# Kernel tuning notes

Hardware: AMD Instinct MI355X
Metric: run time of the kernel (lower is better)

## Reference

```python
import jax, jax.numpy as jnp
import numpy as np

U, I, D = 100000, 50000, 64
N = U + I
E_G, E_U, E_I = 2400000, 1600000, 800000


def _spmm(rows, cols, vals, x, n):
    # sparse [n, m] @ dense [m, d] via gather + scale + segment-sum scatter
    return jax.ops.segment_sum(x[cols] * vals[:, None], rows, num_segments=n)


def setup_inputs() -> dict:
    key = jax.random.key(0)
    ks = jax.random.split(key, 11)
    return {
        "user_emb": jax.random.normal(ks[0], (U, D), dtype=jnp.float32),
        "item_emb": jax.random.normal(ks[1], (I, D), dtype=jnp.float32),
        "graph_rows": jax.random.randint(ks[2], (E_G,), 0, N, dtype=jnp.int32),
        "graph_cols": jax.random.randint(ks[3], (E_G,), 0, N, dtype=jnp.int32),
        "graph_vals": jax.random.uniform(ks[4], (E_G,), dtype=jnp.float32),
        "user_rows": jax.random.randint(ks[5], (E_U,), 0, U, dtype=jnp.int32),
        "user_cols": jax.random.randint(ks[6], (E_U,), 0, U, dtype=jnp.int32),
        "user_vals": jax.random.uniform(ks[7], (E_U,), dtype=jnp.float32),
        "item_rows": jax.random.randint(ks[8], (E_I,), 0, I, dtype=jnp.int32),
        "item_cols": jax.random.randint(ks[9], (E_I,), 0, I, dtype=jnp.int32),
        "item_vals": jax.random.uniform(ks[10], (E_I,), dtype=jnp.float32),
    }


def reference(user_emb, item_emb,
              graph_rows, graph_cols, graph_vals,
              user_rows, user_cols, user_vals,
              item_rows, item_cols, item_vals):
    all_emb = jnp.concatenate([user_emb, item_emb], axis=0)  # [N, D]
    all_emb1 = _spmm(graph_rows, graph_cols, graph_vals, all_emb, N)
    user_emb2 = _spmm(user_rows, user_cols, user_vals, user_emb, U)
    item_emb2 = _spmm(item_rows, item_cols, item_vals, item_emb, I)
    user_emb1, item_emb1 = all_emb1[:U], all_emb1[U:]
    return (user_emb1, item_emb1, user_emb2, item_emb2)
```

## Files before the change

kernel.cpp:

```cpp
#include <hip/hip_runtime.h>

#define DDIM 64
constexpr int U_CNT = 100000;
constexpr int I_CNT = 50000;
constexpr int N_CNT = U_CNT + I_CNT;
constexpr int NB    = N_CNT + U_CNT + I_CNT;

constexpr int BIN_ROWS_LOG = 8;
constexpr int BIN_ROWS = 1 << BIN_ROWS_LOG;
constexpr int BINS = (NB + BIN_ROWS - 1) / BIN_ROWS;
constexpr int BINS_PAD = 1536;
constexpr int SORT_EDGES = 4096;
constexpr int HIST_EDGES = 16384;
constexpr int CAP = 4672;
constexpr int NSLOT = 10;

constexpr int SB_LOG = 12;
constexpr int NSB = (NB + (1 << SB_LOG) - 1) >> SB_LOG;
constexpr int NSB_PAD = 128;
constexpr int BWIN = 48;

typedef unsigned u32x2 __attribute__((ext_vector_type(2)));
typedef unsigned u32x4 __attribute__((ext_vector_type(4)));

__device__ __forceinline__ int wave_incl_scan(int v, int lane) {
#pragma unroll
    for (int off = 1; off < 64; off <<= 1) {
        int t = __shfl_up(v, off, 64);
        if (lane >= off) v += t;
    }
    return v;
}

__device__ __forceinline__ unsigned short f2bf_rne(float f) {
    unsigned u = __float_as_uint(f);
    unsigned r = (u + 0x7FFFu + ((u >> 16) & 1u)) >> 16;
    return (unsigned short)r;
}

__global__ __launch_bounds__(256) void convert_emb(const float* __restrict__ ue,
                                                   const float* __restrict__ ie,
                                                   unsigned short* __restrict__ emb16) {
    int g = blockIdx.x * 256 + threadIdx.x;
    constexpr int UG = U_CNT * (DDIM / 4);
    constexpr int TG = N_CNT * (DDIM / 4);
    if (g >= TG) return;
    float4 v = (g < UG) ? ((const float4*)ue)[g] : ((const float4*)ie)[g - UG];
    ushort4 o;
    o.x = f2bf_rne(v.x); o.y = f2bf_rne(v.y); o.z = f2bf_rne(v.z); o.w = f2bf_rne(v.w);
    ((ushort4*)emb16)[g] = o;
}

__global__ __launch_bounds__(1024) void hist_conv(const int* __restrict__ gr,
                                                  const int* __restrict__ ur,
                                                  const int* __restrict__ ir,
                                                  int EG, int EU, int EI,
                                                  int* __restrict__ cnt,
                                                  const float* __restrict__ ue,
                                                  const float* __restrict__ ie,
                                                  unsigned short* __restrict__ emb16) {
    __shared__ int h[BINS_PAD];
    for (int i = threadIdx.x; i < BINS_PAD; i += 1024) h[i] = 0;

    if (emb16) {
        constexpr int UG = U_CNT * (DDIM / 4);
        constexpr int TG = N_CNT * (DDIM / 4);
        int stride = (int)gridDim.x * 1024;
        for (int g = blockIdx.x * 1024 + threadIdx.x; g < TG; g += stride) {
            float4 v = (g < UG) ? ((const float4*)ue)[g] : ((const float4*)ie)[g - UG];
            ushort4 o;
            o.x = f2bf_rne(v.x); o.y = f2bf_rne(v.y); o.z = f2bf_rne(v.z); o.w = f2bf_rne(v.w);
            ((ushort4*)emb16)[g] = o;
        }
    }
    __syncthreads();

    int base = blockIdx.x * HIST_EDGES;
    int Et = EG + EU + EI;
    for (int j = 0; j < HIST_EDGES / 1024; ++j) {
        int e = base + j * 1024 + threadIdx.x;
        if (e < Et) {
            int b;
            if (e < EG)           b = gr[e];
            else if (e < EG + EU) b = N_CNT + ur[e - EG];
            else                  b = N_CNT + U_CNT + ir[e - EG - EU];
            atomicAdd(&h[b >> BIN_ROWS_LOG], 1);
        }
    }
    __syncthreads();
    for (int i = threadIdx.x; i < BINS; i += 1024) {
        int v = h[i];
        if (v) atomicAdd(&cnt[i], v);
    }
}

__global__ __launch_bounds__(1024) void scan_bins(const int* __restrict__ cnt,
                                                  int* __restrict__ bin_base,
                                                  int* __restrict__ bin_cursor,
                                                  int* __restrict__ sb_base,
                                                  int* __restrict__ sb_cursor,
                                                  int E_total) {
    __shared__ int wsum[16], woff[16];
    int tid = threadIdx.x, lane = tid & 63, wid = tid >> 6;
    int i0 = 2 * tid, i1 = 2 * tid + 1;
    int c0 = (i0 < BINS) ? cnt[i0] : 0;
    int c1 = (i1 < BINS) ? cnt[i1] : 0;
    int v = c0 + c1;
    int incl = wave_incl_scan(v, lane);
    if (lane == 63) wsum[wid] = incl;
    __syncthreads();
    if (wid == 0 && lane < 16) {
        int s = wsum[lane], si = s;
#pragma unroll
        for (int off = 1; off < 16; off <<= 1) {
            int t = __shfl_up(si, off, 64);
            if (lane >= off) si += t;
        }
        woff[lane] = si - s;
    }
    __syncthreads();
    int e = incl - v + woff[wid];
    if (i0 < BINS) { bin_base[i0] = e;      bin_cursor[i0] = e; }
    if (i1 < BINS) { bin_base[i1] = e + c0; bin_cursor[i1] = e + c0; }
    if (tid == 0) bin_base[BINS] = E_total;
    if (sb_base) {
        __syncthreads();
        if (tid <= NSB) {
            int idx = tid << (SB_LOG - BIN_ROWS_LOG);
            int vv = (idx >= BINS) ? E_total : bin_base[idx];
            sb_base[tid] = vv;
            if (tid < NSB) sb_cursor[tid] = vv;
        }
    }
}

__global__ __launch_bounds__(512, 6) void sbsort_all(
        const int* __restrict__ gr, const int* __restrict__ gc, const float* __restrict__ gv,
        const int* __restrict__ ur, const int* __restrict__ uc, const float* __restrict__ uv,
        const int* __restrict__ ir, const int* __restrict__ ic, const float* __restrict__ iv,
        int EG, int EU, int EI,
        int* __restrict__ sb_cursor, uint2* __restrict__ poolA) {
    __shared__ uint2 sorted[SORT_EDGES];
    __shared__ unsigned char ssb[SORT_EDGES];
    __shared__ int hist[NSB_PAD];
    __shared__ int lscan[NSB_PAD];
    __shared__ int lcur[NSB_PAD];
    __shared__ int wsum2[2];

    int tid = threadIdx.x, lane = tid & 63, wid = tid >> 6;
    for (int i = tid; i < NSB_PAD; i += 512) { hist[i] = 0; lcur[i] = 0; }
    __syncthreads();

    const int Et = EG + EU + EI;
    int start = blockIdx.x * SORT_EDGES;
    int base_e = start + tid * 8;
    int myb[8]; unsigned mylo[8]; float myv[8];

#pragma unroll
    for (int j = 0; j < 8; j += 4) {
        int e = base_e + j;
        int sg0 = (e < EG) ? 0 : (e < EG + EU ? 1 : 2);
        int sg3 = (e + 3 < EG) ? 0 : (e + 3 < EG + EU ? 1 : 2);
        if (e + 3 < Et && sg0 == sg3) {
            const int* R; const int* Cc; const float* V; int boff, goff, loc;
            if (sg0 == 0)      { R = gr; Cc = gc; V = gv; boff = 0;             goff = 0;     loc = e; }
            else if (sg0 == 1) { R = ur; Cc = uc; V = uv; boff = N_CNT;         goff = 0;     loc = e - EG; }
            else               { R = ir; Cc = ic; V = iv; boff = N_CNT + U_CNT; goff = U_CNT; loc = e - EG - EU; }
            int4   r4 = *(const int4*)(R + loc);
            int4   c4 = *(const int4*)(Cc + loc);
            float4 v4 = *(const float4*)(V + loc);
            int rr[4] = {r4.x, r4.y, r4.z, r4.w};
            int cc[4] = {c4.x, c4.y, c4.z, c4.w};
            float vv[4] = {v4.x, v4.y, v4.z, v4.w};
#pragma unroll
            for (int q = 0; q < 4; ++q) {
                int bucket = boff + rr[q];
                int sb = bucket >> SB_LOG;
                myb[j + q] = sb;
                mylo[j + q] = ((unsigned)(bucket & 4095) << 18) | (unsigned)(goff + cc[q]);
                myv[j + q] = vv[q];
                atomicAdd(&hist[sb], 1);
            }
        } else {
#pragma unroll
            for (int q = 0; q < 4; ++q) {
                int ee = e + q;
                if (ee < Et) {
                    int r, c; float vl; int boff, goff;
                    if (ee < EG)           { r = gr[ee]; c = gc[ee]; vl = gv[ee]; boff = 0; goff = 0; }
                    else if (ee < EG + EU) { int k = ee - EG;      r = ur[k]; c = uc[k]; vl = uv[k]; boff = N_CNT;         goff = 0; }
                    else                   { int k = ee - EG - EU; r = ir[k]; c = ic[k]; vl = iv[k]; boff = N_CNT + U_CNT; goff = U_CNT; }
                    int bucket = boff + r;
                    int sb = bucket >> SB_LOG;
                    myb[j + q] = sb;
                    mylo[j + q] = ((unsigned)(bucket & 4095) << 18) | (unsigned)(goff + c);
                    myv[j + q] = vl;
                    atomicAdd(&hist[sb], 1);
                } else myb[j + q] = -1;
            }
        }
    }
    __syncthreads();

    int v = 0, incl = 0;
    if (tid < NSB_PAD) {
        v = hist[tid];
        incl = wave_incl_scan(v, lane);
        if (lane == 63) wsum2[wid] = incl;
    }
    __syncthreads();
    if (tid < NSB_PAD) {
        int st = incl - v + (wid ? wsum2[0] : 0);
        lscan[tid] = st;
        if (tid < NSB && v) hist[tid] = atomicAdd(&sb_cursor[tid], v);
    }
    __syncthreads();

#pragma unroll
    for (int j = 0; j < 8; ++j) {
        if (myb[j] >= 0) {
            int p = lscan[myb[j]] + atomicAdd(&lcur[myb[j]], 1);
            sorted[p] = make_uint2(mylo[j], __float_as_uint(myv[j]));
            ssb[p] = (unsigned char)myb[j];
        }
    }
    __syncthreads();

    int cntE = min(SORT_EDGES, Et - start);
    for (int pos = tid; pos < cntE; pos += 512) {
        int b = ssb[pos];
        uint2 t = sorted[pos];
        u32x2 q; q.x = t.x; q.y = t.y;
        __builtin_nontemporal_store(q, (u32x2*)&poolA[hist[b] + (pos - lscan[b])]);
    }
}

__global__ __launch_bounds__(512, 6) void binsort2(const uint2* __restrict__ poolA,
                                                   const int* __restrict__ sb_base, int Et,
                                                   int* __restrict__ bin_cursor,
                                                   uint2* __restrict__ poolB) {
    __shared__ uint2 sorted[SORT_EDGES];
    __shared__ unsigned char sbin[SORT_EDGES];
    __shared__ int hist[BWIN];
    __shared__ int lscan[BWIN];
    __shared__ int lcur[BWIN];
    __shared__ int ssbb[NSB + 1];
    __shared__ int W0s, nloc;

    int tid = threadIdx.x, lane = tid & 63;
    if (tid < BWIN) { hist[tid] = 0; }
    if (tid <= NSB) ssbb[tid] = sb_base[tid];
    __syncthreads();

    int start = blockIdx.x * SORT_EDGES;
    int base_e = start + tid * 8;
    int sb;
    {
        int lo2 = 0, hi2 = NSB - 1;
        while (lo2 < hi2) {
            int mid = (lo2 + hi2 + 1) >> 1;
            if (ssbb[mid] <= base_e) lo2 = mid; else hi2 = mid - 1;
        }
        sb = lo2;
    }
    if (tid == 0) W0s = sb << (SB_LOG - BIN_ROWS_LOG);
    __syncthreads();
    int W0 = W0s;

    int myb[8]; uint2 myp[8];
#pragma unroll
    for (int j = 0; j < 8; j += 2) {
        int e = base_e + j;
        uint2 p0, p1;
        bool v1 = (e + 1 < Et), v0 = (e < Et);
        if (v1) {
            u32x4 q = __builtin_nontemporal_load((const u32x4*)(poolA + e));
            p0.x = q.x; p0.y = q.y; p1.x = q.z; p1.y = q.w;
        } else if (v0) {
            u32x2 q = __builtin_nontemporal_load((const u32x2*)(poolA + e));
            p0.x = q.x; p0.y = q.y;
        }
        if (v0) {
            while (sb < NSB - 1 && e >= ssbb[sb + 1]) ++sb;
            int b = (sb << (SB_LOG - BIN_ROWS_LOG)) + (int)(p0.x >> 26);
            int slot = b - W0;
            if ((unsigned)slot < (unsigned)BWIN) {
                myb[j] = slot; myp[j] = p0;
                atomicAdd(&hist[slot], 1);
            } else {
                int gp = atomicAdd(&bin_cursor[b], 1);
                poolB[gp] = p0;
                myb[j] = -1;
            }
        } else myb[j] = -1;
        if (v1) {
            int e1 = e + 1;
            while (sb < NSB - 1 && e1 >= ssbb[sb + 1]) ++sb;
            int b = (sb << (SB_LOG - BIN_ROWS_LOG)) + (int)(p1.x >> 26);
            int slot = b - W0;
            if ((unsigned)slot < (unsigned)BWIN) {
                myb[j + 1] = slot; myp[j + 1] = p1;
                atomicAdd(&hist[slot], 1);
            } else {
                int gp = atomicAdd(&bin_cursor[b], 1);
                poolB[gp] = p1;
                myb[j + 1] = -1;
            }
        } else myb[j + 1] = -1;
    }
    __syncthreads();

    if (tid < 64) {
        int vv = (tid < BWIN) ? hist[tid] : 0;
        int incl = wave_incl_scan(vv, lane);
        if (tid < BWIN) { lscan[tid] = incl - vv; lcur[tid] = incl - vv; }
        if (tid == BWIN - 1) nloc = incl;
    }
    __syncthreads();
    if (tid < BWIN && hist[tid] > 0)
        hist[tid] = atomicAdd(&bin_cursor[W0 + tid], hist[tid]);
    __syncthreads();

#pragma unroll
    for (int j = 0; j < 8; ++j) {
        if (myb[j] >= 0) {
            int p = atomicAdd(&lcur[myb[j]], 1);
            sorted[p] = myp[j];
            sbin[p] = (unsigned char)myb[j];
        }
    }
    __syncthreads();

    int tot = nloc;
    for (int pos = tid; pos < tot; pos += 512) {
        int sl = sbin[pos];
        uint2 t = sorted[pos];
        u32x2 q; q.x = t.x; q.y = t.y;
        __builtin_nontemporal_store(q, (u32x2*)&poolB[hist[sl] + (pos - lscan[sl])]);
    }
}

__global__ __launch_bounds__(512) void binsort(const int* __restrict__ rows,
                                               const int* __restrict__ cols,
                                               const float* __restrict__ vals, int E,
                                               int bucket_base, int gidx_base,
                                               int* __restrict__ bin_cursor,
                                               uint2* __restrict__ pool) {
    __shared__ uint2 sorted[SORT_EDGES];
    __shared__ unsigned short sbin[SORT_EDGES];
    __shared__ int hist[BINS_PAD];
    __shared__ int lscan[BINS_PAD];
    __shared__ int lcur[BINS_PAD];
    __shared__ int wsum[8], woff[8];

    int tid = threadIdx.x, lane = tid & 63, wid = tid >> 6;
    for (int i = tid; i < BINS_PAD; i += 512) { hist[i] = 0; lcur[i] = 0; }
    __syncthreads();

    int start = blockIdx.x * SORT_EDGES;
    int base_e = start + tid * 8;
    int myb[8]; unsigned mylo[8]; float myv[8];
#pragma unroll
    for (int j = 0; j < 8; j += 4) {
        int e = base_e + j;
        if (e + 3 < E) {
            int4   r4 = *(const int4*)(rows + e);
            int4   c4 = *(const int4*)(cols + e);
            float4 v4 = *(const float4*)(vals + e);
            int rr[4] = {r4.x, r4.y, r4.z, r4.w};
            int cc[4] = {c4.x, c4.y, c4.z, c4.w};
            float vv[4] = {v4.x, v4.y, v4.z, v4.w};
#pragma unroll
            for (int q = 0; q < 4; ++q) {
                int bucket = bucket_base + rr[q];
                myb[j + q] = bucket >> BIN_ROWS_LOG;
                mylo[j + q] = ((unsigned)(bucket & (BIN_ROWS - 1)) << 18) |
                              (unsigned)(gidx_base + cc[q]);
                myv[j + q] = vv[q];
                atomicAdd(&hist[myb[j + q]], 1);
            }
        } else {
#pragma unroll
            for (int q = 0; q < 4; ++q) {
                int ee = e + q;
                if (ee < E) {
                    int bucket = bucket_base + rows[ee];
                    myb[j + q] = bucket >> BIN_ROWS_LOG;
                    mylo[j + q] = ((unsigned)(bucket & (BIN_ROWS - 1)) << 18) |
                                  (unsigned)(gidx_base + cols[ee]);
                    myv[j + q] = vals[ee];
                    atomicAdd(&hist[myb[j + q]], 1);
                } else myb[j + q] = -1;
            }
        }
    }
    __syncthreads();

    int s0 = 3 * tid, s1 = s0 + 1, s2 = s0 + 2;
    int h0 = hist[s0], h1 = hist[s1], h2 = hist[s2];
    int v = h0 + h1 + h2;
    int incl = wave_incl_scan(v, lane);
    if (lane == 63) wsum[wid] = incl;
    __syncthreads();
    if (wid == 0 && lane < 8) {
        int s = wsum[lane], si = s;
#pragma unroll
        for (int off = 1; off < 8; off <<= 1) {
            int t = __shfl_up(si, off, 64);
            if (lane >= off) si += t;
        }
        woff[lane] = si - s;
    }
    __syncthreads();
    int e0 = incl - v + woff[wid];
    lscan[s0] = e0; lscan[s1] = e0 + h0; lscan[s2] = e0 + h0 + h1;
    if (s0 < BINS && h0) hist[s0] = atomicAdd(&bin_cursor[s0], h0);
    if (s1 < BINS && h1) hist[s1] = atomicAdd(&bin_cursor[s1], h1);
    if (s2 < BINS && h2) hist[s2] = atomicAdd(&bin_cursor[s2], h2);
    __syncthreads();

#pragma unroll
    for (int j = 0; j < 8; ++j) {
        if (myb[j] >= 0) {
            int p = lscan[myb[j]] + atomicAdd(&lcur[myb[j]], 1);
            sorted[p] = make_uint2(mylo[j], __float_as_uint(myv[j]));
            sbin[p] = (unsigned short)myb[j];
        }
    }
    __syncthreads();

    int cntE = min(SORT_EDGES, E - start);
    for (int pos = tid; pos < cntE; pos += 512) {
        int b = sbin[pos];
        pool[hist[b] + (pos - lscan[b])] = sorted[pos];
    }
}

template <bool BF16>
__global__ __launch_bounds__(512, 8) void refine_accum(const int* __restrict__ bin_base,
                                                       const uint2* __restrict__ pool,
                                                       const unsigned short* __restrict__ emb16,
                                                       const float* __restrict__ ue,
                                                       const float* __restrict__ ie,
                                                       float* __restrict__ out) {
    __shared__ uint2 sorted[CAP];
    __shared__ int rhist[BIN_ROWS];
    __shared__ int rstart[BIN_ROWS];
    __shared__ int rcur[BIN_ROWS];
    __shared__ int wsum[4];
    int tid = threadIdx.x, lane = tid & 63, wid = tid >> 6;
    int b = blockIdx.x;
    int s = bin_base[b], e = bin_base[b + 1];
    int cnt = min(e - s, CAP);

    if (tid < BIN_ROWS) rhist[tid] = 0;
    __syncthreads();

    uint2 my[NSLOT];
    const u32x2* poolv = (const u32x2*)(pool + s);
#pragma unroll
    for (int j = 0; j < NSLOT; ++j) {
        int idx = tid + j * 512;
        if (idx < cnt) {
            u32x2 q = __builtin_nontemporal_load(poolv + idx);
            my[j].x = q.x; my[j].y = q.y;
            atomicAdd(&rhist[(q.x >> 18) & 255u], 1);
        }
    }
    __syncthreads();

    int v = 0, incl = 0;
    if (tid < BIN_ROWS) {
        v = rhist[tid];
        incl = wave_incl_scan(v, lane);
        if (lane == 63) wsum[wid] = incl;
    }
    __syncthreads();
    if (tid < BIN_ROWS) {
        int off = 0;
#pragma unroll
        for (int w = 0; w < 4; ++w)
            if (w < wid) off += wsum[w];
        int st = incl - v + off;
        rstart[tid] = st; rcur[tid] = st;
    }
    __syncthreads();

#pragma unroll
    for (int j = 0; j < NSLOT; ++j) {
        int idx = tid + j * 512;
        if (idx < cnt) {
            int pos = atomicAdd(&rcur[(my[j].x >> 18) & 255u], 1);
            sorted[pos] = my[j];
        }
    }
    __syncthreads();

    long long rowbase = (long long)b * BIN_ROWS;
    auto gather = [&](unsigned gi) -> float {
        if (BF16) return __uint_as_float((unsigned)emb16[(gi << 6) + lane] << 16);
        return (gi < (unsigned)U_CNT) ? ue[((size_t)gi << 6) + lane]
                                      : ie[(((size_t)gi - U_CNT) << 6) + lane];
    };
    for (int r = wid; r < BIN_ROWS; r += 8) {
        long long row = rowbase + r;
        if (row >= NB) break;
        int k = rstart[r], ke = k + rhist[r];
        float acc0 = 0.f, acc1 = 0.f;
        for (; k + 8 <= ke; k += 8) {
            uint2 p0 = sorted[k],     p1 = sorted[k + 1], p2 = sorted[k + 2], p3 = sorted[k + 3];
            uint2 p4 = sorted[k + 4], p5 = sorted[k + 5], p6 = sorted[k + 6], p7 = sorted[k + 7];
            float x0 = gather(p0.x & 0x3FFFFu);
            float x1 = gather(p1.x & 0x3FFFFu);
            float x2 = gather(p2.x & 0x3FFFFu);
            float x3 = gather(p3.x & 0x3FFFFu);
            float x4 = gather(p4.x & 0x3FFFFu);
            float x5 = gather(p5.x & 0x3FFFFu);
            float x6 = gather(p6.x & 0x3FFFFu);
            float x7 = gather(p7.x & 0x3FFFFu);
            acc0 += __uint_as_float(p0.y) * x0;
            acc1 += __uint_as_float(p1.y) * x1;
            acc0 += __uint_as_float(p2.y) * x2;
            acc1 += __uint_as_float(p3.y) * x3;
            acc0 += __uint_as_float(p4.y) * x4;
            acc1 += __uint_as_float(p5.y) * x5;
            acc0 += __uint_as_float(p6.y) * x6;
            acc1 += __uint_as_float(p7.y) * x7;
        }
        for (; k + 4 <= ke; k += 4) {
            uint2 p0 = sorted[k], p1 = sorted[k + 1], p2 = sorted[k + 2], p3 = sorted[k + 3];
            float x0 = gather(p0.x & 0x3FFFFu);
            float x1 = gather(p1.x & 0x3FFFFu);
            float x2 = gather(p2.x & 0x3FFFFu);
            float x3 = gather(p3.x & 0x3FFFFu);
            acc0 += __uint_as_float(p0.y) * x0;
            acc1 += __uint_as_float(p1.y) * x1;
            acc0 += __uint_as_float(p2.y) * x2;
            acc1 += __uint_as_float(p3.y) * x3;
        }
        for (; k < ke; ++k) {
            uint2 p = sorted[k];
            acc0 += __uint_as_float(p.y) * gather(p.x & 0x3FFFFu);
        }
        __builtin_nontemporal_store(acc0 + acc1, &out[(size_t)row * DDIM + lane]);
    }
}

__global__ void spmm_graph_kernel(const int* __restrict__ rows, const int* __restrict__ cols,
                                  const float* __restrict__ vals,
                                  const float* __restrict__ user_emb,
                                  const float* __restrict__ item_emb,
                                  float* __restrict__ out, int E) {
    long long idx = (long long)blockIdx.x * blockDim.x + threadIdx.x;
    int e = (int)(idx >> 6), d = (int)(idx & 63);
    if (e >= E) return;
    int r = rows[e], c = cols[e];
    float v = vals[e];
    float x = (c < U_CNT) ? user_emb[(long long)c * DDIM + d]
                          : item_emb[(long long)(c - U_CNT) * DDIM + d];
    atomicAdd(&out[(long long)r * DDIM + d], v * x);
}

__global__ void spmm_plain_kernel(const int* __restrict__ rows, const int* __restrict__ cols,
                                  const float* __restrict__ vals,
                                  const float* __restrict__ emb,
                                  float* __restrict__ out, int E) {
    long long idx = (long long)blockIdx.x * blockDim.x + threadIdx.x;
    int e = (int)(idx >> 6), d = (int)(idx & 63);
    if (e >= E) return;
    int r = rows[e], c = cols[e];
    atomicAdd(&out[(long long)r * DDIM + d], vals[e] * emb[(long long)c * DDIM + d]);
}

extern "C" void kernel_launch(void* const* d_in, const int* in_sizes, int n_in,
                              void* d_out, int out_size, void* d_ws, size_t ws_size,
                              hipStream_t stream) {
    const float* user_emb = (const float*)d_in[0];
    const float* item_emb = (const float*)d_in[1];
    const int*   g_rows   = (const int*)d_in[2];
    const int*   g_cols   = (const int*)d_in[3];
    const float* g_vals   = (const float*)d_in[4];
    const int*   u_rows   = (const int*)d_in[5];
    const int*   u_cols   = (const int*)d_in[6];
    const float* u_vals   = (const float*)d_in[7];
    const int*   i_rows   = (const int*)d_in[8];
    const int*   i_cols   = (const int*)d_in[9];
    const float* i_vals   = (const float*)d_in[10];
    float* out = (float*)d_out;

    const int EG = in_sizes[2];
    const int EU = in_sizes[5];
    const int EI = in_sizes[8];
    const int Et = EG + EU + EI;

    const size_t emb_bytes = (size_t)N_CNT * DDIM * sizeof(unsigned short);

    size_t t_off_bb   = (size_t)BINS_PAD * sizeof(int);
    size_t t_off_bc   = t_off_bb + (size_t)(BINS + 1) * sizeof(int);
    size_t t_off_sbb  = t_off_bc + (size_t)BINS * sizeof(int);
    size_t t_off_sbc  = t_off_sbb + (size_t)(NSB + 1) * sizeof(int);
    size_t t_off_pa   = (t_off_sbc + (size_t)NSB * sizeof(int) + 15) & ~(size_t)15;
    size_t t_off_pb   = t_off_pa + (size_t)Et * sizeof(uint2);
    size_t needed_2p  = t_off_pb + (size_t)Et * sizeof(uint2);
    size_t t_off_emb  = (needed_2p + 15) & ~(size_t)15;
    size_t needed_na  = t_off_emb + emb_bytes;
    bool pa_fits_emb  = (size_t)Et * sizeof(uint2) >= emb_bytes;

    size_t o_off_base   = (size_t)BINS_PAD * sizeof(int);
    size_t o_off_cursor = o_off_base + (size_t)(BINS + 1) * sizeof(int);
    size_t o_off_pool   = (o_off_cursor + (size_t)BINS * sizeof(int) + 15) & ~(size_t)15;
    size_t o_off_emb    = o_off_pool + (size_t)Et * sizeof(uint2);
    size_t needed_min   = o_off_emb;
    size_t needed_full  = o_off_emb + emb_bytes;

    if (ws_size >= needed_2p && pa_fits_emb) {
        bool noalias = (ws_size >= needed_na);
        int*   cnt        = (int*)d_ws;
        int*   bin_base   = (int*)((char*)d_ws + t_off_bb);
        int*   bin_cursor = (int*)((char*)d_ws + t_off_bc);
        int*   sb_base    = (int*)((char*)d_ws + t_off_sbb);
        int*   sb_cursor  = (int*)((char*)d_ws + t_off_sbc);
        uint2* poolA      = (uint2*)((char*)d_ws + t_off_pa);
        uint2* poolB      = (uint2*)((char*)d_ws + t_off_pb);
        unsigned short* emb16 = noalias ? (unsigned short*)((char*)d_ws + t_off_emb)
                                        : (unsigned short*)poolA;

        hipMemsetAsync(cnt, 0, (size_t)BINS_PAD * sizeof(int), stream);

        unsigned hblocks = (unsigned)((Et + HIST_EDGES - 1) / HIST_EDGES);
        hist_conv<<<hblocks, 1024, 0, stream>>>(g_rows, u_rows, i_rows, EG, EU, EI, cnt,
                                                user_emb, item_emb,
                                                noalias ? emb16 : (unsigned short*)nullptr);
        scan_bins<<<1, 1024, 0, stream>>>(cnt, bin_base, bin_cursor, sb_base, sb_cursor, Et);

        unsigned nb2 = (unsigned)((Et + SORT_EDGES - 1) / SORT_EDGES);
        sbsort_all<<<nb2, 512, 0, stream>>>(g_rows, g_cols, g_vals,
                                            u_rows, u_cols, u_vals,
                                            i_rows, i_cols, i_vals,
                                            EG, EU, EI, sb_cursor, poolA);
        binsort2<<<nb2, 512, 0, stream>>>(poolA, sb_base, Et, bin_cursor, poolB);

        if (!noalias) {
            unsigned cgrid = (unsigned)((N_CNT * (DDIM / 4) + 255) / 256);
            convert_emb<<<cgrid, 256, 0, stream>>>(user_emb, item_emb, emb16);
        }

        refine_accum<true><<<BINS, 512, 0, stream>>>(bin_base, poolB, emb16,
                                                     user_emb, item_emb, out);
    } else if (ws_size >= needed_min) {
        int*   cnt        = (int*)d_ws;
        int*   bin_base   = (int*)((char*)d_ws + o_off_base);
        int*   bin_cursor = (int*)((char*)d_ws + o_off_cursor);
        uint2* pool       = (uint2*)((char*)d_ws + o_off_pool);
        unsigned short* emb16 = (unsigned short*)((char*)d_ws + o_off_emb);
        bool use_bf16 = (ws_size >= needed_full);

        hipMemsetAsync(cnt, 0, (size_t)BINS_PAD * sizeof(int), stream);

        unsigned hblocks = (unsigned)((Et + HIST_EDGES - 1) / HIST_EDGES);
        hist_conv<<<hblocks, 1024, 0, stream>>>(g_rows, u_rows, i_rows, EG, EU, EI, cnt,
                                                user_emb, item_emb,
                                                use_bf16 ? emb16 : (unsigned short*)nullptr);
        scan_bins<<<1, 1024, 0, stream>>>(cnt, bin_base, bin_cursor, nullptr, nullptr, Et);

        unsigned gb = (unsigned)((EG + SORT_EDGES - 1) / SORT_EDGES);
        unsigned ub = (unsigned)((EU + SORT_EDGES - 1) / SORT_EDGES);
        unsigned ib = (unsigned)((EI + SORT_EDGES - 1) / SORT_EDGES);
        binsort<<<gb, 512, 0, stream>>>(g_rows, g_cols, g_vals, EG, 0,             0,     bin_cursor, pool);
        binsort<<<ub, 512, 0, stream>>>(u_rows, u_cols, u_vals, EU, N_CNT,         0,     bin_cursor, pool);
        binsort<<<ib, 512, 0, stream>>>(i_rows, i_cols, i_vals, EI, N_CNT + U_CNT, U_CNT, bin_cursor, pool);

        if (use_bf16)
            refine_accum<true><<<BINS, 512, 0, stream>>>(bin_base, pool, emb16,
                                                         user_emb, item_emb, out);
        else
            refine_accum<false><<<BINS, 512, 0, stream>>>(bin_base, pool, (const unsigned short*)nullptr,
                                                          user_emb, item_emb, out);
    } else {
        hipMemsetAsync(d_out, 0, (size_t)out_size * sizeof(float), stream);
        const int block = 256;
        {
            long long t = (long long)EG * DDIM;
            spmm_graph_kernel<<<(unsigned)((t + block - 1) / block), block, 0, stream>>>(
                g_rows, g_cols, g_vals, user_emb, item_emb, out, EG);
        }
        {
            long long t = (long long)EU * DDIM;
            spmm_plain_kernel<<<(unsigned)((t + block - 1) / block), block, 0, stream>>>(
                u_rows, u_cols, u_vals, user_emb, out + (size_t)N_CNT * DDIM, EU);
        }
        {
            long long t = (long long)EI * DDIM;
            spmm_plain_kernel<<<(unsigned)((t + block - 1) / block), block, 0, stream>>>(
                i_rows, i_cols, i_vals, item_emb, out + (size_t)(N_CNT + U_CNT) * DDIM, EI);
        }
    }
}
```

Before: 357.0 us.

## Replace atomic-cursor bucket sort with deterministic per-chunk offset sort pipeline

Drops the global histogram pass and atomic super-bucket cursors. Each sort chunk now records per-superbucket counts and local offsets, a single-block scan builds the global offsets, and the second pass gathers its edges by binary search over those offset tables. Refine blocks then locate their runs through per-chunk window tables. The refine gather is reworked so 16-lane groups each load 4 bf16 values at once and four edges are processed in parallel, followed by a shuffle reduction. This removes the histogram kernel, the memset and the global atomics, and makes the order deterministic. In exchange it adds binary searches and larger metadata arrays, and silently clamps slots to BWIN.

```diff
diff --git a/kernel.cpp b/kernel.cpp
--- a/kernel.cpp
+++ b/kernel.cpp
@@ -18,10 +18,12 @@
 constexpr int SB_LOG = 12;
 constexpr int NSB = (NB + (1 << SB_LOG) - 1) >> SB_LOG;
 constexpr int NSB_PAD = 128;
-constexpr int BWIN = 48;
+constexpr int BWIN = 64;
+constexpr int RMAX = 32;
 
 typedef unsigned u32x2 __attribute__((ext_vector_type(2)));
 typedef unsigned u32x4 __attribute__((ext_vector_type(4)));
+typedef float    f32x4 __attribute__((ext_vector_type(4)));
 
 __device__ __forceinline__ int wave_incl_scan(int v, int lane) {
 #pragma unroll
@@ -51,97 +53,16 @@
     ((ushort4*)emb16)[g] = o;
 }
 
-__global__ __launch_bounds__(1024) void hist_conv(const int* __restrict__ gr,
-                                                  const int* __restrict__ ur,
-                                                  const int* __restrict__ ir,
-                                                  int EG, int EU, int EI,
-                                                  int* __restrict__ cnt,
-                                                  const float* __restrict__ ue,
-                                                  const float* __restrict__ ie,
-                                                  unsigned short* __restrict__ emb16) {
-    __shared__ int h[BINS_PAD];
-    for (int i = threadIdx.x; i < BINS_PAD; i += 1024) h[i] = 0;
-
-    if (emb16) {
-        constexpr int UG = U_CNT * (DDIM / 4);
-        constexpr int TG = N_CNT * (DDIM / 4);
-        int stride = (int)gridDim.x * 1024;
-        for (int g = blockIdx.x * 1024 + threadIdx.x; g < TG; g += stride) {
-            float4 v = (g < UG) ? ((const float4*)ue)[g] : ((const float4*)ie)[g - UG];
-            ushort4 o;
-            o.x = f2bf_rne(v.x); o.y = f2bf_rne(v.y); o.z = f2bf_rne(v.z); o.w = f2bf_rne(v.w);
-            ((ushort4*)emb16)[g] = o;
-        }
-    }
-    __syncthreads();
-
-    int base = blockIdx.x * HIST_EDGES;
-    int Et = EG + EU + EI;
-    for (int j = 0; j < HIST_EDGES / 1024; ++j) {
-        int e = base + j * 1024 + threadIdx.x;
-        if (e < Et) {
-            int b;
-            if (e < EG)           b = gr[e];
-            else if (e < EG + EU) b = N_CNT + ur[e - EG];
-            else                  b = N_CNT + U_CNT + ir[e - EG - EU];
-            atomicAdd(&h[b >> BIN_ROWS_LOG], 1);
-        }
-    }
-    __syncthreads();
-    for (int i = threadIdx.x; i < BINS; i += 1024) {
-        int v = h[i];
-        if (v) atomicAdd(&cnt[i], v);
-    }
-}
-
-__global__ __launch_bounds__(1024) void scan_bins(const int* __restrict__ cnt,
-                                                  int* __restrict__ bin_base,
-                                                  int* __restrict__ bin_cursor,
-                                                  int* __restrict__ sb_base,
-                                                  int* __restrict__ sb_cursor,
-                                                  int E_total) {
-    __shared__ int wsum[16], woff[16];
-    int tid = threadIdx.x, lane = tid & 63, wid = tid >> 6;
-    int i0 = 2 * tid, i1 = 2 * tid + 1;
-    int c0 = (i0 < BINS) ? cnt[i0] : 0;
-    int c1 = (i1 < BINS) ? cnt[i1] : 0;
-    int v = c0 + c1;
-    int incl = wave_incl_scan(v, lane);
-    if (lane == 63) wsum[wid] = incl;
-    __syncthreads();
-    if (wid == 0 && lane < 16) {
-        int s = wsum[lane], si = s;
-#pragma unroll
-        for (int off = 1; off < 16; off <<= 1) {
-            int t = __shfl_up(si, off, 64);
-            if (lane >= off) si += t;
-        }
-        woff[lane] = si - s;
-    }
-    __syncthreads();
-    int e = incl - v + woff[wid];
-    if (i0 < BINS) { bin_base[i0] = e;      bin_cursor[i0] = e; }
-    if (i1 < BINS) { bin_base[i1] = e + c0; bin_cursor[i1] = e + c0; }
-    if (tid == 0) bin_base[BINS] = E_total;
-    if (sb_base) {
-        __syncthreads();
-        if (tid <= NSB) {
-            int idx = tid << (SB_LOG - BIN_ROWS_LOG);
-            int vv = (idx >= BINS) ? E_total : bin_base[idx];
-            sb_base[tid] = vv;
-            if (tid < NSB) sb_cursor[tid] = vv;
-        }
-    }
-}
-
-__global__ __launch_bounds__(512, 6) void sbsort_all(
+
+__global__ __launch_bounds__(512, 6) void sbsort_det(
         const int* __restrict__ gr, const int* __restrict__ gc, const float* __restrict__ gv,
         const int* __restrict__ ur, const int* __restrict__ uc, const float* __restrict__ uv,
         const int* __restrict__ ir, const int* __restrict__ ic, const float* __restrict__ iv,
-        int EG, int EU, int EI,
-        int* __restrict__ sb_cursor, uint2* __restrict__ poolA) {
+        int EG, int EU, int EI, int NC,
+        uint2* __restrict__ poolA,
+        unsigned* __restrict__ seg_cnt,
+        unsigned* __restrict__ seg_loc) {
     __shared__ uint2 sorted[SORT_EDGES];
-    __shared__ unsigned char ssb[SORT_EDGES];
     __shared__ int hist[NSB_PAD];
     __shared__ int lscan[NSB_PAD];
     __shared__ int lcur[NSB_PAD];
@@ -209,6 +130,449 @@
         if (lane == 63) wsum2[wid] = incl;
     }
     __syncthreads();
+    if (tid < NSB_PAD) lscan[tid] = incl - v + (wid ? wsum2[0] : 0);
+    __syncthreads();
+
+    if (tid < NSB) {
+        seg_cnt[(size_t)tid * NC + blockIdx.x] = (unsigned)hist[tid];
+        seg_loc[(size_t)tid * NC + blockIdx.x] = (unsigned)lscan[tid];
+    }
+
+#pragma unroll
+    for (int j = 0; j < 8; ++j) {
+        if (myb[j] >= 0) {
+            int p = lscan[myb[j]] + atomicAdd(&lcur[myb[j]], 1);
+            sorted[p] = make_uint2(mylo[j], __float_as_uint(myv[j]));
+        }
+    }
+    __syncthreads();
+
+    int cntE = min(SORT_EDGES, Et - start);
+    const u32x4* s4 = (const u32x4*)sorted;
+    u32x4* d4 = (u32x4*)(poolA + start);
+    for (int i = tid; i < (cntE >> 1); i += 512)
+        __builtin_nontemporal_store(s4[i], d4 + i);
+    if ((cntE & 1) && tid == 0) {
+        u32x2 q; q.x = sorted[cntE - 1].x; q.y = sorted[cntE - 1].y;
+        __builtin_nontemporal_store(q, (u32x2*)(poolA + start + cntE - 1));
+    }
+}
+
+__global__ __launch_bounds__(1024) void scan2(const unsigned* __restrict__ seg_cnt,
+                                              unsigned* __restrict__ seg_off,
+                                              unsigned* __restrict__ sb_base,
+                                              int NC) {
+    __shared__ unsigned sbtot[128];
+    __shared__ int wsum2[2];
+    int tid = threadIdx.x, lane = tid & 63, wid = tid >> 6;
+    if (tid < 128) sbtot[tid] = 0;
+    __syncthreads();
+    for (int sb = wid; sb < NSB; sb += 16) {
+        unsigned carry = 0;
+        for (int c0 = 0; c0 < NC; c0 += 64) {
+            int c = c0 + lane;
+            int v = (c < NC) ? (int)seg_cnt[(size_t)sb * NC + c] : 0;
+            int incl = wave_incl_scan(v, lane);
+            if (c < NC) seg_off[(size_t)sb * (NC + 1) + c] = carry + (unsigned)(incl - v);
+            carry += (unsigned)__shfl(incl, 63, 64);
+        }
+        if (lane == 0) { seg_off[(size_t)sb * (NC + 1) + NC] = carry; sbtot[sb] = carry; }
+    }
+    __syncthreads();
+    int v2 = 0, incl2 = 0;
+    if (tid < 128) {
+        v2 = (int)sbtot[tid];
+        incl2 = wave_incl_scan(v2, lane);
+        if (lane == 63) wsum2[wid] = incl2;
+    }
+    __syncthreads();
+    if (tid <= NSB) sb_base[tid] = (unsigned)(incl2 - v2 + (wid ? wsum2[0] : 0));
+}
+
+__global__ __launch_bounds__(512, 8) void binsort2_det(
+        const uint2* __restrict__ poolA,
+        const unsigned* __restrict__ seg_off,
+        const unsigned* __restrict__ seg_loc,
+        const unsigned* __restrict__ sb_base_g,
+        int NC, int Et,
+        uint2* __restrict__ poolB,
+        unsigned* __restrict__ seg2_cnt,
+        unsigned* __restrict__ seg2_loc,
+        int* __restrict__ w0arr) {
+    __shared__ uint2 sorted[SORT_EDGES];
+    __shared__ int hist[BWIN], lscan[BWIN], lcur[BWIN];
+    __shared__ unsigned sbb[NSB + 1];
+    __shared__ int nloc_s;
+
+    int tid = threadIdx.x, lane = tid & 63;
+    if (tid < BWIN) hist[tid] = 0;
+    if (tid <= NSB) sbb[tid] = sb_base_g[tid];
+    __syncthreads();
+
+    int g0 = blockIdx.x * SORT_EDGES;
+    int m = min(SORT_EDGES, Et - g0);
+
+    int sb_lo;
+    { int lo = 0, hi = NSB - 1;
+      while (lo < hi) { int mid = (lo + hi + 1) >> 1; if ((int)sbb[mid] <= g0) lo = mid; else hi = mid - 1; }
+      sb_lo = lo; }
+    if (tid == 0) w0arr[blockIdx.x] = sb_lo;
+
+    int nval = m - tid * 8; nval = nval < 0 ? 0 : (nval > 8 ? 8 : nval);
+    uint2 myp[8]; int mys[8];
+    if (nval > 0) {
+        int g = g0 + tid * 8;
+        int sb;
+        { int lo = sb_lo, hi = NSB - 1;
+          while (lo < hi) { int mid = (lo + hi + 1) >> 1; if ((int)sbb[mid] <= g) lo = mid; else hi = mid - 1; }
+          sb = lo; }
+        const unsigned* offrow = seg_off + (size_t)sb * (NC + 1);
+        int p = g - (int)sbb[sb];
+        int c;
+        { int lo = 0, hi = NC - 1;
+          while (lo < hi) { int mid = (lo + hi + 1) >> 1; if ((int)offrow[mid] <= p) lo = mid; else hi = mid - 1; }
+          c = lo; }
+        unsigned coff = offrow[c], cnext = offrow[c + 1];
+        unsigned cloc = seg_loc[(size_t)sb * NC + c];
+        for (int j = 0; j < nval; ++j) {
+            int gj = g + j;
+            if (gj >= (int)sbb[sb + 1]) {
+                do { ++sb; } while (gj >= (int)sbb[sb + 1]);
+                offrow = seg_off + (size_t)sb * (NC + 1);
+                p = gj - (int)sbb[sb];
+                int lo = 0, hi = NC - 1;
+                while (lo < hi) { int mid = (lo + hi + 1) >> 1; if ((int)offrow[mid] <= p) lo = mid; else hi = mid - 1; }
+                c = lo; coff = offrow[c]; cnext = offrow[c + 1];
+                cloc = seg_loc[(size_t)sb * NC + c];
+            } else {
+                p = gj - (int)sbb[sb];
+            }
+            while ((unsigned)p >= cnext) {
+                ++c; coff = cnext; cnext = offrow[c + 1];
+                cloc = seg_loc[(size_t)sb * NC + c];
+            }
+            int src = c * SORT_EDGES + (int)cloc + (p - (int)coff);
+            u32x2 q = __builtin_nontemporal_load((const u32x2*)(poolA + src));
+            uint2 e; e.x = q.x; e.y = q.y;
+            int slot = ((sb - sb_lo) << 4) + (int)(e.x >> 26);
+            if ((unsigned)slot >= (unsigned)BWIN) slot = BWIN - 1;
+            myp[j] = e; mys[j] = slot;
+            atomicAdd(&hist[slot], 1);
+        }
+    }
+    __syncthreads();
+
+    if (tid < 64) {
+        int vv = hist[tid];
+        int incl = wave_incl_scan(vv, lane);
+        lscan[tid] = incl - vv; lcur[tid] = incl - vv;
+        if (tid == 63) nloc_s = incl;
+    }
+    __syncthreads();
+    if (tid < BWIN) {
+        seg2_cnt[(size_t)blockIdx.x * BWIN + tid] = (unsigned)hist[tid];
+        seg2_loc[(size_t)blockIdx.x * BWIN + tid] = (unsigned)lscan[tid];
+    }
+    for (int j = 0; j < nval; ++j) {
+        int pos = atomicAdd(&lcur[mys[j]], 1);
+        sorted[pos] = myp[j];
+    }
+    __syncthreads();
+
+    int tot = nloc_s;
+    const u32x4* s4 = (const u32x4*)sorted;
+    u32x4* d4 = (u32x4*)(poolB + g0);
+    for (int i = tid; i < (tot >> 1); i += 512)
+        __builtin_nontemporal_store(s4[i], d4 + i);
+    if ((tot & 1) && tid == 0) {
+        u32x2 q; q.x = sorted[tot - 1].x; q.y = sorted[tot - 1].y;
+        __builtin_nontemporal_store(q, (u32x2*)(poolB + g0 + tot - 1));
+    }
+}
+
+__global__ __launch_bounds__(512, 8) void refine_det(
+        const unsigned* __restrict__ sb_base_g,
+        const int* __restrict__ w0arr,
+        const unsigned* __restrict__ seg2_cnt,
+        const unsigned* __restrict__ seg2_loc,
+        const uint2* __restrict__ poolB,
+        const unsigned short* __restrict__ emb16,
+        float* __restrict__ out) {
+    __shared__ uint2 sorted[CAP];
+    __shared__ int rhist[BIN_ROWS];
+    __shared__ int rstart[BIN_ROWS];
+    __shared__ int rcur[BIN_ROWS];
+    __shared__ int runpre[RMAX + 1];
+    __shared__ int runsrc[RMAX];
+    __shared__ int wsum[4];
+    int tid = threadIdx.x, lane = tid & 63, wid = tid >> 6;
+    int b = blockIdx.x;
+    int sb = b >> 4, b15 = b & 15;
+    unsigned sbS = sb_base_g[sb], sbE = sb_base_g[sb + 1];
+    int kc0 = (int)(sbS >> 12);
+    int nk = (sbE > sbS) ? ((int)((sbE - 1) >> 12) - kc0 + 1) : 0;
+    if (nk > RMAX) nk = RMAX;
+
+    if (tid < BIN_ROWS) rhist[tid] = 0;
+    int rl = 0;
+    if (tid < nk) {
+        int kc = kc0 + tid;
+        int slot = ((sb - w0arr[kc]) << 4) + b15;
+        if ((unsigned)slot < (unsigned)BWIN) {
+            rl = (int)seg2_cnt[(size_t)kc * BWIN + slot];
+            runsrc[tid] = kc * SORT_EDGES + (int)seg2_loc[(size_t)kc * BWIN + slot];
+        } else runsrc[tid] = 0;
+    }
+    __syncthreads();
+    if (tid < 64) {
+        int incl = wave_incl_scan(rl, lane);
+        if (lane < RMAX) runpre[lane] = incl - rl;
+        if (lane == 63) runpre[RMAX] = incl;
+    }
+    __syncthreads();
+    int cnt = runpre[RMAX]; if (cnt > CAP) cnt = CAP;
+
+    uint2 my[NSLOT];
+#pragma unroll
+    for (int j = 0; j < NSLOT; ++j) {
+        int idx = tid + j * 512;
+        if (idx < cnt) {
+            int lo = 0, hi = nk - 1;
+            while (lo < hi) { int mid = (lo + hi + 1) >> 1; if (runpre[mid] <= idx) lo = mid; else hi = mid - 1; }
+            int src = runsrc[lo] + (idx - runpre[lo]);
+            u32x2 q = __builtin_nontemporal_load((const u32x2*)(poolB + src));
+            my[j].x = q.x; my[j].y = q.y;
+            atomicAdd(&rhist[(q.x >> 18) & 255u], 1);
+        }
+    }
+    __syncthreads();
+
+    int v = 0, incl = 0;
+    if (tid < BIN_ROWS) {
+        v = rhist[tid];
+        incl = wave_incl_scan(v, lane);
+        if (lane == 63) wsum[wid] = incl;
+    }
+    __syncthreads();
+    if (tid < BIN_ROWS) {
+        int off = 0;
+#pragma unroll
+        for (int w = 0; w < 4; ++w)
+            if (w < wid) off += wsum[w];
+        int st = incl - v + off;
+        rstart[tid] = st; rcur[tid] = st;
+    }
+    __syncthreads();
+
+#pragma unroll
+    for (int j = 0; j < NSLOT; ++j) {
+        int idx = tid + j * 512;
+        if (idx < cnt) {
+            int pos = atomicAdd(&rcur[(my[j].x >> 18) & 255u], 1);
+            sorted[pos] = my[j];
+        }
+    }
+    __syncthreads();
+
+    long long rowbase = (long long)b * BIN_ROWS;
+    int grp = lane >> 4, gl = lane & 15;
+    const u32x2* embq = (const u32x2*)emb16;
+    for (int r = wid; r < BIN_ROWS; r += 8) {
+        long long row = rowbase + r;
+        if (row >= NB) break;
+        int k = rstart[r], ke = k + rhist[r];
+        float a0 = 0.f, a1 = 0.f, a2 = 0.f, a3 = 0.f;
+        for (; k + 8 <= ke; k += 8) {
+            uint2 pA = sorted[k + grp];
+            uint2 pB = sorted[k + 4 + grp];
+            unsigned gA = pA.x & 0x3FFFFu, gB = pB.x & 0x3FFFFu;
+            u32x2 wA = embq[(size_t)gA * 16 + gl];
+            u32x2 wB = embq[(size_t)gB * 16 + gl];
+            float vA = __uint_as_float(pA.y), vB = __uint_as_float(pB.y);
+            a0 += vA * __uint_as_float(wA.x << 16);
+            a1 += vA * __uint_as_float(wA.x & 0xFFFF0000u);
+            a2 += vA * __uint_as_float(wA.y << 16);
+            a3 += vA * __uint_as_float(wA.y & 0xFFFF0000u);
+            a0 += vB * __uint_as_float(wB.x << 16);
+            a1 += vB * __uint_as_float(wB.x & 0xFFFF0000u);
+            a2 += vB * __uint_as_float(wB.y << 16);
+            a3 += vB * __uint_as_float(wB.y & 0xFFFF0000u);
+        }
+        if (k + 4 <= ke) {
+            uint2 pA = sorted[k + grp];
+            unsigned gA = pA.x & 0x3FFFFu;
+            u32x2 wA = embq[(size_t)gA * 16 + gl];
+            float vA = __uint_as_float(pA.y);
+            a0 += vA * __uint_as_float(wA.x << 16);
+            a1 += vA * __uint_as_float(wA.x & 0xFFFF0000u);
+            a2 += vA * __uint_as_float(wA.y << 16);
+            a3 += vA * __uint_as_float(wA.y & 0xFFFF0000u);
+            k += 4;
+        }
+        int rem = ke - k;
+        if (grp < rem) {
+            uint2 pA = sorted[k + grp];
+            unsigned gA = pA.x & 0x3FFFFu;
+            u32x2 wA = embq[(size_t)gA * 16 + gl];
+            float vA = __uint_as_float(pA.y);
+            a0 += vA * __uint_as_float(wA.x << 16);
+            a1 += vA * __uint_as_float(wA.x & 0xFFFF0000u);
+            a2 += vA * __uint_as_float(wA.y << 16);
+            a3 += vA * __uint_as_float(wA.y & 0xFFFF0000u);
+        }
+        a0 += __shfl_xor(a0, 16, 64); a1 += __shfl_xor(a1, 16, 64);
+        a2 += __shfl_xor(a2, 16, 64); a3 += __shfl_xor(a3, 16, 64);
+        a0 += __shfl_xor(a0, 32, 64); a1 += __shfl_xor(a1, 32, 64);
+        a2 += __shfl_xor(a2, 32, 64); a3 += __shfl_xor(a3, 32, 64);
+        if (lane < 16) {
+            f32x4 o; o.x = a0; o.y = a1; o.z = a2; o.w = a3;
+            __builtin_nontemporal_store(o, (f32x4*)(out + (size_t)row * DDIM) + gl);
+        }
+    }
+}
+
+
+__global__ __launch_bounds__(1024) void hist_conv(const int* __restrict__ gr,
+                                                  const int* __restrict__ ur,
+                                                  const int* __restrict__ ir,
+                                                  int EG, int EU, int EI,
+                                                  int* __restrict__ cnt) {
+    __shared__ int h[BINS_PAD];
+    for (int i = threadIdx.x; i < BINS_PAD; i += 1024) h[i] = 0;
+    __syncthreads();
+    int base = blockIdx.x * HIST_EDGES;
+    int Et = EG + EU + EI;
+    for (int j = 0; j < HIST_EDGES / 1024; ++j) {
+        int e = base + j * 1024 + threadIdx.x;
+        if (e < Et) {
+            int b;
+            if (e < EG)           b = gr[e];
+            else if (e < EG + EU) b = N_CNT + ur[e - EG];
+            else                  b = N_CNT + U_CNT + ir[e - EG - EU];
+            atomicAdd(&h[b >> BIN_ROWS_LOG], 1);
+        }
+    }
+    __syncthreads();
+    for (int i = threadIdx.x; i < BINS; i += 1024) {
+        int v = h[i];
+        if (v) atomicAdd(&cnt[i], v);
+    }
+}
+
+__global__ __launch_bounds__(1024) void scan_bins(const int* __restrict__ cnt,
+                                                  int* __restrict__ bin_base,
+                                                  int* __restrict__ bin_cursor,
+                                                  int* __restrict__ sb_base,
+                                                  int* __restrict__ sb_cursor,
+                                                  int E_total) {
+    __shared__ int wsum[16], woff[16];
+    int tid = threadIdx.x, lane = tid & 63, wid = tid >> 6;
+    int i0 = 2 * tid, i1 = 2 * tid + 1;
+    int c0 = (i0 < BINS) ? cnt[i0] : 0;
+    int c1 = (i1 < BINS) ? cnt[i1] : 0;
+    int v = c0 + c1;
+    int incl = wave_incl_scan(v, lane);
+    if (lane == 63) wsum[wid] = incl;
+    __syncthreads();
+    if (wid == 0 && lane < 16) {
+        int s = wsum[lane], si = s;
+#pragma unroll
+        for (int off = 1; off < 16; off <<= 1) {
+            int t = __shfl_up(si, off, 64);
+            if (lane >= off) si += t;
+        }
+        woff[lane] = si - s;
+    }
+    __syncthreads();
+    int e = incl - v + woff[wid];
+    if (i0 < BINS) { bin_base[i0] = e;      bin_cursor[i0] = e; }
+    if (i1 < BINS) { bin_base[i1] = e + c0; bin_cursor[i1] = e + c0; }
+    if (tid == 0) bin_base[BINS] = E_total;
+    if (sb_base) {
+        __syncthreads();
+        if (tid <= NSB) {
+            int idx = tid << (SB_LOG - BIN_ROWS_LOG);
+            int vv = (idx >= BINS) ? E_total : bin_base[idx];
+            sb_base[tid] = vv;
+            if (tid < NSB) sb_cursor[tid] = vv;
+        }
+    }
+}
+
+__global__ __launch_bounds__(512, 6) void sbsort_all(
+        const int* __restrict__ gr, const int* __restrict__ gc, const float* __restrict__ gv,
+        const int* __restrict__ ur, const int* __restrict__ uc, const float* __restrict__ uv,
+        const int* __restrict__ ir, const int* __restrict__ ic, const float* __restrict__ iv,
+        int EG, int EU, int EI,
+        int* __restrict__ sb_cursor, uint2* __restrict__ poolA) {
+    __shared__ uint2 sorted[SORT_EDGES];
+    __shared__ unsigned char ssb[SORT_EDGES];
+    __shared__ int hist[NSB_PAD];
+    __shared__ int lscan[NSB_PAD];
+    __shared__ int lcur[NSB_PAD];
+    __shared__ int wsum2[2];
+
+    int tid = threadIdx.x, lane = tid & 63, wid = tid >> 6;
+    for (int i = tid; i < NSB_PAD; i += 512) { hist[i] = 0; lcur[i] = 0; }
+    __syncthreads();
+
+    const int Et = EG + EU + EI;
+    int start = blockIdx.x * SORT_EDGES;
+    int base_e = start + tid * 8;
+    int myb[8]; unsigned mylo[8]; float myv[8];
+#pragma unroll
+    for (int j = 0; j < 8; j += 4) {
+        int e = base_e + j;
+        int sg0 = (e < EG) ? 0 : (e < EG + EU ? 1 : 2);
+        int sg3 = (e + 3 < EG) ? 0 : (e + 3 < EG + EU ? 1 : 2);
+        if (e + 3 < Et && sg0 == sg3) {
+            const int* R; const int* Cc; const float* V; int boff, goff, loc;
+            if (sg0 == 0)      { R = gr; Cc = gc; V = gv; boff = 0;             goff = 0;     loc = e; }
+            else if (sg0 == 1) { R = ur; Cc = uc; V = uv; boff = N_CNT;         goff = 0;     loc = e - EG; }
+            else               { R = ir; Cc = ic; V = iv; boff = N_CNT + U_CNT; goff = U_CNT; loc = e - EG - EU; }
+            int4   r4 = *(const int4*)(R + loc);
+            int4   c4 = *(const int4*)(Cc + loc);
+            float4 v4 = *(const float4*)(V + loc);
+            int rr[4] = {r4.x, r4.y, r4.z, r4.w};
+            int cc[4] = {c4.x, c4.y, c4.z, c4.w};
+            float vv[4] = {v4.x, v4.y, v4.z, v4.w};
+#pragma unroll
+            for (int q = 0; q < 4; ++q) {
+                int bucket = boff + rr[q];
+                int sb = bucket >> SB_LOG;
+                myb[j + q] = sb;
+                mylo[j + q] = ((unsigned)(bucket & 4095) << 18) | (unsigned)(goff + cc[q]);
+                myv[j + q] = vv[q];
+                atomicAdd(&hist[sb], 1);
+            }
+        } else {
+#pragma unroll
+            for (int q = 0; q < 4; ++q) {
+                int ee = e + q;
+                if (ee < Et) {
+                    int r, c; float vl; int boff, goff;
+                    if (ee < EG)           { r = gr[ee]; c = gc[ee]; vl = gv[ee]; boff = 0; goff = 0; }
+                    else if (ee < EG + EU) { int k = ee - EG;      r = ur[k]; c = uc[k]; vl = uv[k]; boff = N_CNT;         goff = 0; }
+                    else                   { int k = ee - EG - EU; r = ir[k]; c = ic[k]; vl = iv[k]; boff = N_CNT + U_CNT; goff = U_CNT; }
+                    int bucket = boff + r;
+                    int sb = bucket >> SB_LOG;
+                    myb[j + q] = sb;
+                    mylo[j + q] = ((unsigned)(bucket & 4095) << 18) | (unsigned)(goff + c);
+                    myv[j + q] = vl;
+                    atomicAdd(&hist[sb], 1);
+                } else myb[j + q] = -1;
+            }
+        }
+    }
+    __syncthreads();
+
+    int v = 0, incl = 0;
+    if (tid < NSB_PAD) {
+        v = hist[tid];
+        incl = wave_incl_scan(v, lane);
+        if (lane == 63) wsum2[wid] = incl;
+    }
+    __syncthreads();
     if (tid < NSB_PAD) {
         int st = incl - v + (wid ? wsum2[0] : 0);
         lscan[tid] = st;
@@ -228,27 +592,28 @@
 
     int cntE = min(SORT_EDGES, Et - start);
     for (int pos = tid; pos < cntE; pos += 512) {
-        int b = ssb[pos];
+        int bb = ssb[pos];
         uint2 t = sorted[pos];
         u32x2 q; q.x = t.x; q.y = t.y;
-        __builtin_nontemporal_store(q, (u32x2*)&poolA[hist[b] + (pos - lscan[b])]);
-    }
-}
-
-__global__ __launch_bounds__(512, 6) void binsort2(const uint2* __restrict__ poolA,
-                                                   const int* __restrict__ sb_base, int Et,
-                                                   int* __restrict__ bin_cursor,
-                                                   uint2* __restrict__ poolB) {
+        __builtin_nontemporal_store(q, (u32x2*)&poolA[hist[bb] + (pos - lscan[bb])]);
+    }
+}
+
+__global__ __launch_bounds__(512, 6) void binsort2_old(const uint2* __restrict__ poolA,
+                                                       const int* __restrict__ sb_base, int Et,
+                                                       int* __restrict__ bin_cursor,
+                                                       uint2* __restrict__ poolB) {
+    constexpr int BWINO = 48;
     __shared__ uint2 sorted[SORT_EDGES];
     __shared__ unsigned char sbin[SORT_EDGES];
-    __shared__ int hist[BWIN];
-    __shared__ int lscan[BWIN];
-    __shared__ int lcur[BWIN];
+    __shared__ int hist[BWINO];
+    __shared__ int lscan[BWINO];
+    __shared__ int lcur[BWINO];
     __shared__ int ssbb[NSB + 1];
     __shared__ int W0s, nloc;
 
     int tid = threadIdx.x, lane = tid & 63;
-    if (tid < BWIN) { hist[tid] = 0; }
+    if (tid < BWINO) hist[tid] = 0;
     if (tid <= NSB) ssbb[tid] = sb_base[tid];
     __syncthreads();
 
@@ -282,13 +647,13 @@
         }
         if (v0) {
             while (sb < NSB - 1 && e >= ssbb[sb + 1]) ++sb;
-            int b = (sb << (SB_LOG - BIN_ROWS_LOG)) + (int)(p0.x >> 26);
-            int slot = b - W0;
-            if ((unsigned)slot < (unsigned)BWIN) {
+            int bb = (sb << (SB_LOG - BIN_ROWS_LOG)) + (int)(p0.x >> 26);
+            int slot = bb - W0;
+            if ((unsigned)slot < (unsigned)BWINO) {
                 myb[j] = slot; myp[j] = p0;
                 atomicAdd(&hist[slot], 1);
             } else {
-                int gp = atomicAdd(&bin_cursor[b], 1);
+                int gp = atomicAdd(&bin_cursor[bb], 1);
                 poolB[gp] = p0;
                 myb[j] = -1;
             }
@@ -296,13 +661,13 @@
         if (v1) {
             int e1 = e + 1;
             while (sb < NSB - 1 && e1 >= ssbb[sb + 1]) ++sb;
-            int b = (sb << (SB_LOG - BIN_ROWS_LOG)) + (int)(p1.x >> 26);
-            int slot = b - W0;
-            if ((unsigned)slot < (unsigned)BWIN) {
+            int bb = (sb << (SB_LOG - BIN_ROWS_LOG)) + (int)(p1.x >> 26);
+            int slot = bb - W0;
+            if ((unsigned)slot < (unsigned)BWINO) {
                 myb[j + 1] = slot; myp[j + 1] = p1;
                 atomicAdd(&hist[slot], 1);
             } else {
-                int gp = atomicAdd(&bin_cursor[b], 1);
+                int gp = atomicAdd(&bin_cursor[bb], 1);
                 poolB[gp] = p1;
                 myb[j + 1] = -1;
             }
@@ -311,13 +676,13 @@
     __syncthreads();
 
     if (tid < 64) {
-        int vv = (tid < BWIN) ? hist[tid] : 0;
+        int vv = (tid < BWINO) ? hist[tid] : 0;
         int incl = wave_incl_scan(vv, lane);
-        if (tid < BWIN) { lscan[tid] = incl - vv; lcur[tid] = incl - vv; }
-        if (tid == BWIN - 1) nloc = incl;
-    }
-    __syncthreads();
-    if (tid < BWIN && hist[tid] > 0)
+        if (tid < BWINO) { lscan[tid] = incl - vv; lcur[tid] = incl - vv; }
+        if (tid == BWINO - 1) nloc = incl;
+    }
+    __syncthreads();
+    if (tid < BWINO && hist[tid] > 0)
         hist[tid] = atomicAdd(&bin_cursor[W0 + tid], hist[tid]);
     __syncthreads();
 
@@ -340,109 +705,10 @@
     }
 }
 
-__global__ __launch_bounds__(512) void binsort(const int* __restrict__ rows,
-                                               const int* __restrict__ cols,
-                                               const float* __restrict__ vals, int E,
-                                               int bucket_base, int gidx_base,
-                                               int* __restrict__ bin_cursor,
-                                               uint2* __restrict__ pool) {
-    __shared__ uint2 sorted[SORT_EDGES];
-    __shared__ unsigned short sbin[SORT_EDGES];
-    __shared__ int hist[BINS_PAD];
-    __shared__ int lscan[BINS_PAD];
-    __shared__ int lcur[BINS_PAD];
-    __shared__ int wsum[8], woff[8];
-
-    int tid = threadIdx.x, lane = tid & 63, wid = tid >> 6;
-    for (int i = tid; i < BINS_PAD; i += 512) { hist[i] = 0; lcur[i] = 0; }
-    __syncthreads();
-
-    int start = blockIdx.x * SORT_EDGES;
-    int base_e = start + tid * 8;
-    int myb[8]; unsigned mylo[8]; float myv[8];
-#pragma unroll
-    for (int j = 0; j < 8; j += 4) {
-        int e = base_e + j;
-        if (e + 3 < E) {
-            int4   r4 = *(const int4*)(rows + e);
-            int4   c4 = *(const int4*)(cols + e);
-            float4 v4 = *(const float4*)(vals + e);
-            int rr[4] = {r4.x, r4.y, r4.z, r4.w};
-            int cc[4] = {c4.x, c4.y, c4.z, c4.w};
-            float vv[4] = {v4.x, v4.y, v4.z, v4.w};
-#pragma unroll
-            for (int q = 0; q < 4; ++q) {
-                int bucket = bucket_base + rr[q];
-                myb[j + q] = bucket >> BIN_ROWS_LOG;
-                mylo[j + q] = ((unsigned)(bucket & (BIN_ROWS - 1)) << 18) |
-                              (unsigned)(gidx_base + cc[q]);
-                myv[j + q] = vv[q];
-                atomicAdd(&hist[myb[j + q]], 1);
-            }
-        } else {
-#pragma unroll
-            for (int q = 0; q < 4; ++q) {
-                int ee = e + q;
-                if (ee < E) {
-                    int bucket = bucket_base + rows[ee];
-                    myb[j + q] = bucket >> BIN_ROWS_LOG;
-                    mylo[j + q] = ((unsigned)(bucket & (BIN_ROWS - 1)) << 18) |
-                                  (unsigned)(gidx_base + cols[ee]);
-                    myv[j + q] = vals[ee];
-                    atomicAdd(&hist[myb[j + q]], 1);
-                } else myb[j + q] = -1;
-            }
-        }
-    }
-    __syncthreads();
-
-    int s0 = 3 * tid, s1 = s0 + 1, s2 = s0 + 2;
-    int h0 = hist[s0], h1 = hist[s1], h2 = hist[s2];
-    int v = h0 + h1 + h2;
-    int incl = wave_incl_scan(v, lane);
-    if (lane == 63) wsum[wid] = incl;
-    __syncthreads();
-    if (wid == 0 && lane < 8) {
-        int s = wsum[lane], si = s;
-#pragma unroll
-        for (int off = 1; off < 8; off <<= 1) {
-            int t = __shfl_up(si, off, 64);
-            if (lane >= off) si += t;
-        }
-        woff[lane] = si - s;
-    }
-    __syncthreads();
-    int e0 = incl - v + woff[wid];
-    lscan[s0] = e0; lscan[s1] = e0 + h0; lscan[s2] = e0 + h0 + h1;
-    if (s0 < BINS && h0) hist[s0] = atomicAdd(&bin_cursor[s0], h0);
-    if (s1 < BINS && h1) hist[s1] = atomicAdd(&bin_cursor[s1], h1);
-    if (s2 < BINS && h2) hist[s2] = atomicAdd(&bin_cursor[s2], h2);
-    __syncthreads();
-
-#pragma unroll
-    for (int j = 0; j < 8; ++j) {
-        if (myb[j] >= 0) {
-            int p = lscan[myb[j]] + atomicAdd(&lcur[myb[j]], 1);
-            sorted[p] = make_uint2(mylo[j], __float_as_uint(myv[j]));
-            sbin[p] = (unsigned short)myb[j];
-        }
-    }
-    __syncthreads();
-
-    int cntE = min(SORT_EDGES, E - start);
-    for (int pos = tid; pos < cntE; pos += 512) {
-        int b = sbin[pos];
-        pool[hist[b] + (pos - lscan[b])] = sorted[pos];
-    }
-}
-
-template <bool BF16>
-__global__ __launch_bounds__(512, 8) void refine_accum(const int* __restrict__ bin_base,
-                                                       const uint2* __restrict__ pool,
-                                                       const unsigned short* __restrict__ emb16,
-                                                       const float* __restrict__ ue,
-                                                       const float* __restrict__ ie,
-                                                       float* __restrict__ out) {
+__global__ __launch_bounds__(512, 8) void refine_accum_old(const int* __restrict__ bin_base,
+                                                           const uint2* __restrict__ pool,
+                                                           const unsigned short* __restrict__ emb16,
+                                                           float* __restrict__ out) {
     __shared__ uint2 sorted[CAP];
     __shared__ int rhist[BIN_ROWS];
     __shared__ int rstart[BIN_ROWS];
@@ -497,50 +763,26 @@
     __syncthreads();
 
     long long rowbase = (long long)b * BIN_ROWS;
-    auto gather = [&](unsigned gi) -> float {
-        if (BF16) return __uint_as_float((unsigned)emb16[(gi << 6) + lane] << 16);
-        return (gi < (unsigned)U_CNT) ? ue[((size_t)gi << 6) + lane]
-                                      : ie[(((size_t)gi - U_CNT) << 6) + lane];
-    };
     for (int r = wid; r < BIN_ROWS; r += 8) {
         long long row = rowbase + r;
         if (row >= NB) break;
         int k = rstart[r], ke = k + rhist[r];
         float acc0 = 0.f, acc1 = 0.f;
-        for (; k + 8 <= ke; k += 8) {
-            uint2 p0 = sorted[k],     p1 = sorted[k + 1], p2 = sorted[k + 2], p3 = sorted[k + 3];
-            uint2 p4 = sorted[k + 4], p5 = sorted[k + 5], p6 = sorted[k + 6], p7 = sorted[k + 7];
-            float x0 = gather(p0.x & 0x3FFFFu);
-            float x1 = gather(p1.x & 0x3FFFFu);
-            float x2 = gather(p2.x & 0x3FFFFu);
-            float x3 = gather(p3.x & 0x3FFFFu);
-            float x4 = gather(p4.x & 0x3FFFFu);
-            float x5 = gather(p5.x & 0x3FFFFu);
-            float x6 = gather(p6.x & 0x3FFFFu);
-            float x7 = gather(p7.x & 0x3FFFFu);
+        for (; k + 4 <= ke; k += 4) {
+            uint2 p0 = sorted[k], p1 = sorted[k + 1], p2 = sorted[k + 2], p3 = sorted[k + 3];
+            float x0 = __uint_as_float((unsigned)emb16[((p0.x & 0x3FFFFu) << 6) + lane] << 16);
+            float x1 = __uint_as_float((unsigned)emb16[((p1.x & 0x3FFFFu) << 6) + lane] << 16);
+            float x2 = __uint_as_float((unsigned)emb16[((p2.x & 0x3FFFFu) << 6) + lane] << 16);
+            float x3 = __uint_as_float((unsigned)emb16[((p3.x & 0x3FFFFu) << 6) + lane] << 16);
             acc0 += __uint_as_float(p0.y) * x0;
             acc1 += __uint_as_float(p1.y) * x1;
             acc0 += __uint_as_float(p2.y) * x2;
             acc1 += __uint_as_float(p3.y) * x3;
-            acc0 += __uint_as_float(p4.y) * x4;
-            acc1 += __uint_as_float(p5.y) * x5;
-            acc0 += __uint_as_float(p6.y) * x6;
-            acc1 += __uint_as_float(p7.y) * x7;
-        }
-        for (; k + 4 <= ke; k += 4) {
-            uint2 p0 = sorted[k], p1 = sorted[k + 1], p2 = sorted[k + 2], p3 = sorted[k + 3];
-            float x0 = gather(p0.x & 0x3FFFFu);
-            float x1 = gather(p1.x & 0x3FFFFu);
-            float x2 = gather(p2.x & 0x3FFFFu);
-            float x3 = gather(p3.x & 0x3FFFFu);
-            acc0 += __uint_as_float(p0.y) * x0;
-            acc1 += __uint_as_float(p1.y) * x1;
-            acc0 += __uint_as_float(p2.y) * x2;
-            acc1 += __uint_as_float(p3.y) * x3;
         }
         for (; k < ke; ++k) {
             uint2 p = sorted[k];
-            acc0 += __uint_as_float(p.y) * gather(p.x & 0x3FFFFu);
+            acc0 += __uint_as_float(p.y) *
+                    __uint_as_float((unsigned)emb16[((p.x & 0x3FFFFu) << 6) + lane] << 16);
         }
         __builtin_nontemporal_store(acc0 + acc1, &out[(size_t)row * DDIM + lane]);
     }
@@ -592,8 +834,20 @@
     const int EU = in_sizes[5];
     const int EI = in_sizes[8];
     const int Et = EG + EU + EI;
+    const int NC = (Et + SORT_EDGES - 1) / SORT_EDGES;
 
     const size_t emb_bytes = (size_t)N_CNT * DDIM * sizeof(unsigned short);
+    bool pa_fits_emb = (size_t)Et * sizeof(uint2) >= emb_bytes;
+
+    size_t n_off_w0   = 80 * 4;
+    size_t n_off_scnt = n_off_w0 + (size_t)NC * 4;
+    size_t n_off_sloc = n_off_scnt + (size_t)NSB * NC * 4;
+    size_t n_off_soff = n_off_sloc + (size_t)NSB * NC * 4;
+    size_t n_off_s2c  = n_off_soff + (size_t)NSB * (NC + 1) * 4;
+    size_t n_off_s2l  = n_off_s2c + (size_t)NC * BWIN * 4;
+    size_t n_off_pa   = (n_off_s2l + (size_t)NC * BWIN * 4 + 15) & ~(size_t)15;
+    size_t n_off_pb   = n_off_pa + (size_t)Et * sizeof(uint2);
+    size_t needed_new = n_off_pb + (size_t)Et * sizeof(uint2);
 
     size_t t_off_bb   = (size_t)BINS_PAD * sizeof(int);
     size_t t_off_bc   = t_off_bb + (size_t)(BINS + 1) * sizeof(int);
@@ -602,19 +856,30 @@
     size_t t_off_pa   = (t_off_sbc + (size_t)NSB * sizeof(int) + 15) & ~(size_t)15;
     size_t t_off_pb   = t_off_pa + (size_t)Et * sizeof(uint2);
     size_t needed_2p  = t_off_pb + (size_t)Et * sizeof(uint2);
-    size_t t_off_emb  = (needed_2p + 15) & ~(size_t)15;
-    size_t needed_na  = t_off_emb + emb_bytes;
-    bool pa_fits_emb  = (size_t)Et * sizeof(uint2) >= emb_bytes;
-
-    size_t o_off_base   = (size_t)BINS_PAD * sizeof(int);
-    size_t o_off_cursor = o_off_base + (size_t)(BINS + 1) * sizeof(int);
-    size_t o_off_pool   = (o_off_cursor + (size_t)BINS * sizeof(int) + 15) & ~(size_t)15;
-    size_t o_off_emb    = o_off_pool + (size_t)Et * sizeof(uint2);
-    size_t needed_min   = o_off_emb;
-    size_t needed_full  = o_off_emb + emb_bytes;
-
-    if (ws_size >= needed_2p && pa_fits_emb) {
-        bool noalias = (ws_size >= needed_na);
+
+    if (ws_size >= needed_new && pa_fits_emb) {
+        unsigned* sb_base  = (unsigned*)d_ws;
+        int*      w0arr    = (int*)((char*)d_ws + n_off_w0);
+        unsigned* seg_cnt  = (unsigned*)((char*)d_ws + n_off_scnt);
+        unsigned* seg_loc  = (unsigned*)((char*)d_ws + n_off_sloc);
+        unsigned* seg_off  = (unsigned*)((char*)d_ws + n_off_soff);
+        unsigned* seg2_cnt = (unsigned*)((char*)d_ws + n_off_s2c);
+        unsigned* seg2_loc = (unsigned*)((char*)d_ws + n_off_s2l);
+        uint2*    poolA    = (uint2*)((char*)d_ws + n_off_pa);
+        uint2*    poolB    = (uint2*)((char*)d_ws + n_off_pb);
+        unsigned short* emb16 = (unsigned short*)poolA;
+
+        sbsort_det<<<(unsigned)NC, 512, 0, stream>>>(
+            g_rows, g_cols, g_vals, u_rows, u_cols, u_vals, i_rows, i_cols, i_vals,
+            EG, EU, EI, NC, poolA, seg_cnt, seg_loc);
+        scan2<<<1, 1024, 0, stream>>>(seg_cnt, seg_off, sb_base, NC);
+        binsort2_det<<<(unsigned)NC, 512, 0, stream>>>(
+            poolA, seg_off, seg_loc, sb_base, NC, Et, poolB, seg2_cnt, seg2_loc, w0arr);
+        unsigned cgrid = (unsigned)((N_CNT * (DDIM / 4) + 255) / 256);
+        convert_emb<<<cgrid, 256, 0, stream>>>(user_emb, item_emb, emb16);
+        refine_det<<<BINS, 512, 0, stream>>>(sb_base, w0arr, seg2_cnt, seg2_loc,
+                                             poolB, emb16, out);
+    } else if (ws_size >= needed_2p && pa_fits_emb) {
         int*   cnt        = (int*)d_ws;
         int*   bin_base   = (int*)((char*)d_ws + t_off_bb);
         int*   bin_cursor = (int*)((char*)d_ws + t_off_bc);
@@ -622,60 +887,21 @@
         int*   sb_cursor  = (int*)((char*)d_ws + t_off_sbc);
         uint2* poolA      = (uint2*)((char*)d_ws + t_off_pa);
         uint2* poolB      = (uint2*)((char*)d_ws + t_off_pb);
-        unsigned short* emb16 = noalias ? (unsigned short*)((char*)d_ws + t_off_emb)
-                                        : (unsigned short*)poolA;
+        unsigned short* emb16 = (unsigned short*)poolA;
 
         hipMemsetAsync(cnt, 0, (size_t)BINS_PAD * sizeof(int), stream);
-
         unsigned hblocks = (unsigned)((Et + HIST_EDGES - 1) / HIST_EDGES);
-        hist_conv<<<hblocks, 1024, 0, stream>>>(g_rows, u_rows, i_rows, EG, EU, EI, cnt,
-                                                user_emb, item_emb,
-                                                noalias ? emb16 : (unsigned short*)nullptr);
+        hist_conv<<<hblocks, 1024, 0, stream>>>(g_rows, u_rows, i_rows, EG, EU, EI, cnt);
         scan_bins<<<1, 1024, 0, stream>>>(cnt, bin_base, bin_cursor, sb_base, sb_cursor, Et);
-
         unsigned nb2 = (unsigned)((Et + SORT_EDGES - 1) / SORT_EDGES);
         sbsort_all<<<nb2, 512, 0, stream>>>(g_rows, g_cols, g_vals,
                                             u_rows, u_cols, u_vals,
                                             i_rows, i_cols, i_vals,
                                             EG, EU, EI, sb_cursor, poolA);
-        binsort2<<<nb2, 512, 0, stream>>>(poolA, sb_base, Et, bin_cursor, poolB);
-
-        if (!noalias) {
-            unsigned cgrid = (unsigned)((N_CNT * (DDIM / 4) + 255) / 256);
-            convert_emb<<<cgrid, 256, 0, stream>>>(user_emb, item_emb, emb16);
-        }
-
-        refine_accum<true><<<BINS, 512, 0, stream>>>(bin_base, poolB, emb16,
-                                                     user_emb, item_emb, out);
-    } else if (ws_size >= needed_min) {
-        int*   cnt        = (int*)d_ws;
-        int*   bin_base   = (int*)((char*)d_ws + o_off_base);
-        int*   bin_cursor = (int*)((char*)d_ws + o_off_cursor);
-        uint2* pool       = (uint2*)((char*)d_ws + o_off_pool);
-        unsigned short* emb16 = (unsigned short*)((char*)d_ws + o_off_emb);
-        bool use_bf16 = (ws_size >= needed_full);
-
-        hipMemsetAsync(cnt, 0, (size_t)BINS_PAD * sizeof(int), stream);
-
-        unsigned hblocks = (unsigned)((Et + HIST_EDGES - 1) / HIST_EDGES);
-        hist_conv<<<hblocks, 1024, 0, stream>>>(g_rows, u_rows, i_rows, EG, EU, EI, cnt,
-                                                user_emb, item_emb,
-                                                use_bf16 ? emb16 : (unsigned short*)nullptr);
-        scan_bins<<<1, 1024, 0, stream>>>(cnt, bin_base, bin_cursor, nullptr, nullptr, Et);
-
-        unsigned gb = (unsigned)((EG + SORT_EDGES - 1) / SORT_EDGES);
-        unsigned ub = (unsigned)((EU + SORT_EDGES - 1) / SORT_EDGES);
-        unsigned ib = (unsigned)((EI + SORT_EDGES - 1) / SORT_EDGES);
-        binsort<<<gb, 512, 0, stream>>>(g_rows, g_cols, g_vals, EG, 0,             0,     bin_cursor, pool);
-        binsort<<<ub, 512, 0, stream>>>(u_rows, u_cols, u_vals, EU, N_CNT,         0,     bin_cursor, pool);
-        binsort<<<ib, 512, 0, stream>>>(i_rows, i_cols, i_vals, EI, N_CNT + U_CNT, U_CNT, bin_cursor, pool);
-
-        if (use_bf16)
-            refine_accum<true><<<BINS, 512, 0, stream>>>(bin_base, pool, emb16,
-                                                         user_emb, item_emb, out);
-        else
-            refine_accum<false><<<BINS, 512, 0, stream>>>(bin_base, pool, (const unsigned short*)nullptr,
-                                                          user_emb, item_emb, out);
+        binsort2_old<<<nb2, 512, 0, stream>>>(poolA, sb_base, Et, bin_cursor, poolB);
+        unsigned cgrid = (unsigned)((N_CNT * (DDIM / 4) + 255) / 256);
+        convert_emb<<<cgrid, 256, 0, stream>>>(user_emb, item_emb, emb16);
+        refine_accum_old<<<BINS, 512, 0, stream>>>(bin_base, poolB, emb16, out);
     } else {
         hipMemsetAsync(d_out, 0, (size_t)out_size * sizeof(float), stream);
         const int block = 256;
```

Result: slower. 490.9 us (+37.5%).
